# Kernel tuning notes

Hardware: AMD Instinct MI355X
Metric: run time of the kernel (lower is better)

## Reference

```python
import jax, jax.numpy as jnp
import numpy as np

B, S, D_IN = 16, 1024, 1024
H, D_OUT = 16, 128

def setup_inputs() -> dict:
    key = jax.random.key(0)
    k1, k2, k3 = jax.random.split(key, 3)
    x = jax.random.normal(k1, (B, S, D_IN), dtype=jnp.float32)
    W = jax.random.normal(k2, (H, 3, D_IN, D_OUT), dtype=jnp.float32) * (1.0 / np.sqrt(D_IN))
    Wo = jax.random.normal(k3, (H * D_OUT, D_OUT), dtype=jnp.float32) * (1.0 / np.sqrt(H * D_OUT))
    return {"x": x, "W": W, "Wo": Wo}

def reference(x, W, Wo):
    # x: [B,S,D_IN], W: [H,3,D_IN,E], Wo: [H*E,E]
    E = W.shape[-1]
    q = jnp.einsum('bsd,hde->bhse', x, W[:, 0])
    k = jnp.einsum('bsd,hde->bhse', x, W[:, 1])
    v = jnp.einsum('bsd,hde->bhse', x, W[:, 2])
    # NOTE: source divides by (output_dim * 0.5), not sqrt(output_dim)
    scores = jnp.einsum('bhse,bhte->bhst', q, k) / (E * 0.5)
    attn = jax.nn.softmax(scores, axis=-1)
    o = jnp.einsum('bhst,bhte->bhse', attn, v)          # [B,H,S,E]
    o = jnp.transpose(o, (0, 2, 1, 3)).reshape(x.shape[0], x.shape[1], -1)  # concat heads
    return jnp.einsum('bsf,fe->bse', o, Wo)
```

## Files before the change

kernel.cpp:

```cpp
#include <hip/hip_runtime.h>

typedef unsigned short u16;
typedef _Float16 f16;
typedef __attribute__((ext_vector_type(8))) _Float16 half8;
typedef __attribute__((ext_vector_type(8))) short short8;
typedef __attribute__((ext_vector_type(4))) float f32x4;
typedef __attribute__((ext_vector_type(4))) float f4;
typedef __attribute__((ext_vector_type(4))) u16 u16x4;

#define B_ 16
#define S_ 1024
#define DIN_ 1024
#define H_ 16
#define E_ 128

#define EXPK 0.0225546041776533f

__device__ __forceinline__ u16 f2h(float f) {
  f16 h = (f16)f;
  return __builtin_bit_cast(u16, h);
}

__device__ __forceinline__ void gl2lds16(const u16* g, u16* l) {
  __builtin_amdgcn_global_load_lds((const __attribute__((address_space(1))) void*)g,
                                   (__attribute__((address_space(3))) void*)l, 16, 0, 0);
}

__global__ __launch_bounds__(256) void zero_f32(float* __restrict__ p) {
  int i = (blockIdx.x * 256 + threadIdx.x) * 4;
  f4 z = {0.f, 0.f, 0.f, 0.f};
  *reinterpret_cast<f4*>(p + i) = z;
}

__global__ __launch_bounds__(256) void cvt_f32_f16(const float* __restrict__ in,
                                                   u16* __restrict__ out) {
  int i = (blockIdx.x * 256 + threadIdx.x) * 4;
  f4 v = *reinterpret_cast<const f4*>(in + i);
  u16x4 o;
  o[0] = f2h(v[0]); o[1] = f2h(v[1]); o[2] = f2h(v[2]); o[3] = f2h(v[3]);
  *reinterpret_cast<u16x4*>(out + i) = o;
}

__global__ __launch_bounds__(256) void transpose_cvt(const float* __restrict__ in,
                                                     u16* __restrict__ out,
                                                     int R, int C) {
  __shared__ float tile[32][33];
  const size_t moff = (size_t)blockIdx.z * R * C;
  const float* src = in + moff;
  u16* dst = out + moff;
  int c0 = blockIdx.x * 32, r0 = blockIdx.y * 32;
  int tx = threadIdx.x & 31, ty = threadIdx.x >> 5;
#pragma unroll
  for (int i = 0; i < 32; i += 8)
    tile[ty + i][tx] = src[(size_t)(r0 + ty + i) * C + c0 + tx];
  __syncthreads();
#pragma unroll
  for (int i = 0; i < 32; i += 8)
    dst[(size_t)(c0 + ty + i) * R + r0 + tx] = f2h(tile[tx][ty + i]);
}

template<int K>
__global__ __launch_bounds__(512, 2) void gemm256_qkv(const u16* __restrict__ A,
                                                      const u16* __restrict__ BT,
                                                      u16* __restrict__ q, u16* __restrict__ kk,
                                                      u16* __restrict__ vT) {
  constexpr int KT = K / 64;
  const int tid = threadIdx.x;
  const int m0 = blockIdx.x * 256;
  const int nt0 = blockIdx.y;
  const u16* Bblk = BT + (size_t)nt0 * 256 * K;
  __shared__ __align__(16) u16 smem[65536];
  const int w = tid >> 6, lane = tid & 63;
  const int quad = lane >> 4, ln = lane & 15;
  const int wr = w >> 2, wc = w & 3;

  const int srow = tid >> 3;
  const int scc = (tid & 7) ^ (srow & 7);
  const u16* agp = A + (size_t)(m0 + srow) * K + scc * 8;
  const u16* bgp = Bblk + (size_t)srow * K + scc * 8;

#define STAGE256(buf, t)                                                     \
  do {                                                                       \
    u16* ab_ = smem + (buf) * 32768;                                         \
    _Pragma("unroll") for (int i_ = 0; i_ < 4; i_++) {                       \
      gl2lds16(agp + (t) * 64 + (size_t)i_ * 64 * K, ab_ + i_ * 4096 + tid * 8);        \
      gl2lds16(bgp + (t) * 64 + (size_t)i_ * 64 * K, ab_ + 16384 + i_ * 4096 + tid * 8);\
    }                                                                        \
  } while (0)

  int offA[8][2], offB[4][2];
#pragma unroll
  for (int mt = 0; mt < 8; mt++) {
    int row = wr * 128 + mt * 16 + ln;
#pragma unroll
    for (int k2 = 0; k2 < 2; k2++)
      offA[mt][k2] = row * 64 + (((k2 * 4 + quad) ^ (ln & 7)) * 8);
  }
#pragma unroll
  for (int nt = 0; nt < 4; nt++) {
    int row = wc * 64 + nt * 16 + ln;
#pragma unroll
    for (int k2 = 0; k2 < 2; k2++)
      offB[nt][k2] = 16384 + row * 64 + (((k2 * 4 + quad) ^ (ln & 7)) * 8);
  }

  f32x4 acc[8][4];
  f32x4 zero = {0.f, 0.f, 0.f, 0.f};
#pragma unroll
  for (int mt = 0; mt < 8; mt++)
#pragma unroll
    for (int nt = 0; nt < 4; nt++) acc[mt][nt] = zero;

  STAGE256(0, 0);
#pragma unroll
  for (int t = 0; t < KT; t++) {
    asm volatile("s_waitcnt vmcnt(0)" ::: "memory");
    asm volatile("s_barrier" ::: "memory");
    if (t < KT - 1) STAGE256((t + 1) & 1, t + 1);
    const u16* ab = smem + (t & 1) * 32768;
#pragma unroll
    for (int k2 = 0; k2 < 2; k2++) {
      half8 bf[4];
#pragma unroll
      for (int j = 0; j < 4; j++)
        bf[j] = *reinterpret_cast<const half8*>(&ab[offB[j][k2]]);
#pragma unroll
      for (int mh = 0; mh < 2; mh++) {
        half8 af[4];
#pragma unroll
        for (int i = 0; i < 4; i++)
          af[i] = *reinterpret_cast<const half8*>(&ab[offA[mh * 4 + i][k2]]);
        asm volatile("s_barrier" ::: "memory");
        asm volatile("s_waitcnt lgkmcnt(0)" ::: "memory");
        __builtin_amdgcn_sched_barrier(0);
        __builtin_amdgcn_s_setprio(1);
#pragma unroll
        for (int i = 0; i < 4; i++)
#pragma unroll
          for (int j = 0; j < 4; j++)
            acc[mh * 4 + i][j] = __builtin_amdgcn_mfma_f32_16x16x32_f16(
                af[i], bf[j], acc[mh * 4 + i][j], 0, 0, 0);
        __builtin_amdgcn_s_setprio(0);
        asm volatile("s_barrier" ::: "memory");
      }
    }
  }
#undef STAGE256

  __syncthreads();
  const int slab = nt0 * 2 + (wc >> 1);
  const int h = slab / 3, c = slab % 3;
  if (c < 2) {
    u16* dst = (c == 0) ? q : kk;
    const float sc = (c == 0) ? EXPK : 1.0f;
#pragma unroll
    for (int mt = 0; mt < 8; mt++)
#pragma unroll
      for (int nt = 0; nt < 4; nt++)
#pragma unroll
        for (int r = 0; r < 4; r++) {
          int tok = m0 + wr * 128 + mt * 16 + quad * 4 + r;
          int bb = tok >> 10, s = tok & 1023;
          int e = (wc & 1) * 64 + nt * 16 + ln;
          dst[(((size_t)bb * H_ + h) * S_ + s) * E_ + e] = f2h(acc[mt][nt][r] * sc);
        }
  } else {
#pragma unroll
    for (int mt = 0; mt < 8; mt++)
#pragma unroll
      for (int nt = 0; nt < 4; nt++) {
        int tok0 = wr * 128 + mt * 16 + quad * 4;
        int ptok0 = (tok0 & ~31) | ((tok0 & 12) << 1) | ((tok0 & 16) >> 2);
        int e = (wc & 1) * 64 + nt * 16 + ln;
        u16x4 pp;
#pragma unroll
        for (int r = 0; r < 4; r++) pp[r] = f2h(acc[mt][nt][r]);
        *reinterpret_cast<u16x4*>(&smem[e * 260 + ptok0]) = pp;
      }
  }
  __syncthreads();
  int vslab = -1;
  if ((nt0 * 2) % 3 == 2) vslab = 0;
  else if ((nt0 * 2 + 1) % 3 == 2) vslab = 1;
  if (vslab >= 0) {
    const int hv = (nt0 * 2 + vslab) / 3;
    const int bb = m0 >> 10, sbase = m0 & 1023;
    u16* vbase = vT + (((size_t)bb * H_ + hv) * E_) * S_;
#pragma unroll
    for (int i = 0; i < 8; i++) {
      int e = (tid >> 5) + i * 16, s0 = (tid & 31) * 8;
      *reinterpret_cast<short8*>(&vbase[(size_t)e * S_ + sbase + s0]) =
          *reinterpret_cast<const short8*>(&smem[e * 260 + s0]);
    }
  }
}

template<int MODE, int KSPLIT, int K>
__global__ __launch_bounds__(256) void gemm_bt(const u16* __restrict__ A,
                                               const u16* __restrict__ BT,
                                               u16* __restrict__ q, u16* __restrict__ kk,
                                               u16* __restrict__ vT, float* __restrict__ out) {
  const int tid = threadIdx.x;
  const int m0 = blockIdx.x * 128;
  const u16* Bblk = BT + (size_t)blockIdx.y * 128 * K;
  __shared__ __align__(16) u16 smem[132 * 128];
  u16* As = smem;
  u16* Bs = smem + 8192;
  const int w = tid >> 6, lane = tid & 63;
  const int quad = lane >> 4, ln = lane & 15;
  const int wr = w >> 1, wc = w & 1;

  const int kbeg = (KSPLIT > 1) ? blockIdx.z * (K / KSPLIT) : 0;
  constexpr int KLEN = K / KSPLIT;

  const int rr = lane >> 3;
  const int cc = (lane & 7) ^ rr;
  const u16* agp[4];
  const u16* bgp[4];
#pragma unroll
  for (int i = 0; i < 4; i++) {
    int row = i * 32 + w * 8 + rr;
    agp[i] = A + (size_t)(m0 + row) * K + kbeg + cc * 8;
    bgp[i] = Bblk + (size_t)row * K + kbeg + cc * 8;
  }

  int offA[4][2], offB[4][2];
#pragma unroll
  for (int mt = 0; mt < 4; mt++) {
    int row = wr * 64 + mt * 16 + ln;
#pragma unroll
    for (int k2 = 0; k2 < 2; k2++)
      offA[mt][k2] = row * 64 + (((k2 * 4 + quad) ^ (ln & 7)) * 8);
  }
#pragma unroll
  for (int nt = 0; nt < 4; nt++) {
    int row = wc * 64 + nt * 16 + ln;
#pragma unroll
    for (int k2 = 0; k2 < 2; k2++)
      offB[nt][k2] = row * 64 + (((k2 * 4 + quad) ^ (ln & 7)) * 8);
  }

  f32x4 acc[4][4];
  f32x4 zero = {0.f, 0.f, 0.f, 0.f};
#pragma unroll
  for (int mt = 0; mt < 4; mt++)
#pragma unroll
    for (int nt = 0; nt < 4; nt++) acc[mt][nt] = zero;

#pragma unroll
  for (int k0 = 0; k0 < KLEN; k0 += 64) {
    __syncthreads();
#pragma unroll
    for (int i = 0; i < 4; i++) {
      gl2lds16(agp[i] + k0, As + i * 2048 + w * 512);
      gl2lds16(bgp[i] + k0, Bs + i * 2048 + w * 512);
    }
    __syncthreads();
#pragma unroll
    for (int k2 = 0; k2 < 2; k2++) {
      half8 af[4], bfr[4];
#pragma unroll
      for (int mt = 0; mt < 4; mt++)
        af[mt] = *reinterpret_cast<const half8*>(&As[offA[mt][k2]]);
#pragma unroll
      for (int nt = 0; nt < 4; nt++)
        bfr[nt] = *reinterpret_cast<const half8*>(&Bs[offB[nt][k2]]);
#pragma unroll
      for (int mt = 0; mt < 4; mt++)
#pragma unroll
        for (int nt = 0; nt < 4; nt++)
          acc[mt][nt] = __builtin_amdgcn_mfma_f32_16x16x32_f16(af[mt], bfr[nt], acc[mt][nt], 0, 0, 0);
    }
  }

  {
#pragma unroll
    for (int mt = 0; mt < 4; mt++)
#pragma unroll
      for (int nt = 0; nt < 4; nt++)
#pragma unroll
        for (int r = 0; r < 4; r++) {
          int row = wr * 64 + mt * 16 + quad * 4 + r;
          int e = wc * 64 + nt * 16 + ln;
          if (KSPLIT > 1)
            atomicAdd(&out[(size_t)(m0 + row) * E_ + e], acc[mt][nt][r]);
          else
            out[(size_t)(m0 + row) * E_ + e] = acc[mt][nt][r];
        }
  }
}

struct SmemKV {
  u16 ks[64 * 128];
  u16 vs[128 * 64];
};
union SmemAttn {
  u16 qs[128 * 132];
  SmemKV s;
};

__global__ __launch_bounds__(256, 3) void attn_kernel(const u16* __restrict__ qg,
                                                      const u16* __restrict__ kg,
                                                      const u16* __restrict__ vg,
                                                      u16* __restrict__ og) {
  __shared__ __align__(16) SmemAttn sm;
  const int tid = threadIdx.x;
  const int id = blockIdx.x;
  const int g = id >> 6, qt = (id >> 3) & 7, x = id & 7;
  const int hb = g * 8 + x;
  const int b = hb >> 4, h = hb & 15;
  const int q0 = qt * 128;
  const size_t bh = (size_t)(b * H_ + h);
  const u16* qp = qg + bh * S_ * E_;
  const u16* kp = kg + bh * S_ * E_;
  const u16* vp = vg + bh * E_ * S_;
  const int w = tid >> 6, lane = tid & 63, quad = lane >> 4, ln = lane & 15;

#pragma unroll
  for (int i = 0; i < 8; i++) {
    int idx = tid + i * 256;
    int row = idx >> 4, col = (idx & 15) * 8;
    *reinterpret_cast<short8*>(&sm.qs[row * 132 + col]) =
        *reinterpret_cast<const short8*>(&qp[(size_t)(q0 + row) * E_ + col]);
  }
  __syncthreads();
  half8 qf[2][4];
#pragma unroll
  for (int mt = 0; mt < 2; mt++)
#pragma unroll
    for (int ks = 0; ks < 4; ks++)
      qf[mt][ks] = *reinterpret_cast<const half8*>(
          &sm.qs[(w * 32 + mt * 16 + ln) * 132 + ks * 32 + quad * 8]);

  const int krow = w * 4 + (lane >> 4);
  const int kc = ((lane & 15) & 8) | (((lane & 15) & 7) ^ (krow & 7));
  const u16* kbase = kp + (size_t)krow * E_ + kc * 8;
  const int vrow = w * 8 + (lane >> 3);
  const int vc = (lane & 7) ^ ((lane >> 3) & 7);
  const u16* vbase = vp + (size_t)vrow * S_ + vc * 8;

  f32x4 zero = {0.f, 0.f, 0.f, 0.f};
  f32x4 oa[2][8];
#pragma unroll
  for (int mt = 0; mt < 2; mt++)
#pragma unroll
    for (int nt = 0; nt < 8; nt++) oa[mt][nt] = zero;
  float lsum[2] = {0.f, 0.f};

  for (int kt = 0; kt < 16; kt++) {
    __syncthreads();
#pragma unroll
    for (int i = 0; i < 4; i++) {
      gl2lds16(kbase + (size_t)kt * 8192 + i * 16 * E_, &sm.s.ks[(i * 256 + w * 64) * 8]);
      gl2lds16(vbase + (size_t)kt * 64 + i * 32 * S_,   &sm.s.vs[(i * 256 + w * 64) * 8]);
    }
    __syncthreads();

    f32x4 sa[2][4];
#pragma unroll
    for (int mt = 0; mt < 2; mt++)
#pragma unroll
      for (int nt = 0; nt < 4; nt++) sa[mt][nt] = zero;
#pragma unroll
    for (int ks = 0; ks < 4; ks++) {
      half8 kf[4];
#pragma unroll
      for (int nt = 0; nt < 4; nt++) {
        int c = ks * 4 + quad;
        int cs = (c & 8) | ((c & 7) ^ (ln & 7));
        kf[nt] = *reinterpret_cast<const half8*>(&sm.s.ks[(nt * 16 + ln) * 128 + cs * 8]);
      }
#pragma unroll
      for (int mt = 0; mt < 2; mt++)
#pragma unroll
        for (int nt = 0; nt < 4; nt++)
          sa[mt][nt] = __builtin_amdgcn_mfma_f32_16x16x32_f16(kf[nt], qf[mt][ks], sa[mt][nt], 0, 0, 0);
    }

    half8 pfr[2][2];
#pragma unroll
    for (int mt = 0; mt < 2; mt++) {
      float psum = 0.f;
#pragma unroll
      for (int k2 = 0; k2 < 2; k2++) {
        half8 ph;
#pragma unroll
        for (int hhalf = 0; hhalf < 2; hhalf++)
#pragma unroll
          for (int r = 0; r < 4; r++) {
            float p = exp2f(sa[mt][k2 * 2 + hhalf][r]);
            psum += p;
            ph[hhalf * 4 + r] = (f16)p;
          }
        pfr[mt][k2] = ph;
      }
      lsum[mt] += psum;
    }

#pragma unroll
    for (int k2 = 0; k2 < 2; k2++) {
#pragma unroll
      for (int nt8 = 0; nt8 < 8; nt8++) {
        int c = k2 * 4 + quad;
        int cs = c ^ (ln & 7);
        half8 vf = *reinterpret_cast<const half8*>(&sm.s.vs[(nt8 * 16 + ln) * 64 + cs * 8]);
#pragma unroll
        for (int mt = 0; mt < 2; mt++)
          oa[mt][nt8] = __builtin_amdgcn_mfma_f32_16x16x32_f16(pfr[mt][k2], vf, oa[mt][nt8], 0, 0, 0);
      }
    }
  }

#pragma unroll
  for (int mt = 0; mt < 2; mt++) {
    float l = lsum[mt];
    l += __shfl_xor(l, 16);
    l += __shfl_xor(l, 32);
#pragma unroll
    for (int r = 0; r < 4; r++) {
      float lr = __shfl(l, quad * 4 + r);
      float rl = 1.0f / lr;
      int srow = q0 + w * 32 + mt * 16 + quad * 4 + r;
      size_t base = ((size_t)b * S_ + srow) * (H_ * E_) + (size_t)h * E_;
#pragma unroll
      for (int nt8 = 0; nt8 < 8; nt8++)
        og[base + nt8 * 16 + ln] = f2h(oa[mt][nt8][r] * rl);
    }
  }
}

extern "C" void kernel_launch(void* const* d_in, const int* in_sizes, int n_in,
                              void* d_out, int out_size, void* d_ws, size_t ws_size,
                              hipStream_t stream) {
  const float* x = (const float*)d_in[0];
  const float* W = (const float*)d_in[1];
  const float* Wo = (const float*)d_in[2];
  float* out = (float*)d_out;
  char* ws = (char*)d_ws;

  const size_t WBT_BYTES = (size_t)H_ * 3 * DIN_ * E_ * 2;
  const size_t WOT_BYTES = (size_t)H_ * E_ * E_ * 2 * 2;
  const size_t FIXED = WBT_BYTES + WOT_BYTES;

  const size_t XB_PER   = (size_t)S_ * DIN_ * 2;
  const size_t QKV_PER  = (size_t)H_ * S_ * E_ * 2;
  const size_t OB_PER   = (size_t)S_ * H_ * E_ * 2;
  const size_t PER_ITEM = XB_PER + 3 * QKV_PER + OB_PER;

  int Bc = 1;
  for (int c = 16; c >= 1; c >>= 1) {
    if (FIXED + (size_t)c * PER_ITEM <= ws_size) { Bc = c; break; }
  }

  u16* WbT = (u16*)(ws);
  u16* WoT = (u16*)(ws + WBT_BYTES);
  char* cb = ws + FIXED;
  u16* xb  = (u16*)(cb);
  u16* qb  = (u16*)(cb + (size_t)Bc * XB_PER);
  u16* kb  = (u16*)(cb + (size_t)Bc * (XB_PER + QKV_PER));
  u16* vTb = (u16*)(cb + (size_t)Bc * (XB_PER + 2 * QKV_PER));
  u16* ob  = (u16*)(cb + (size_t)Bc * (XB_PER + 3 * QKV_PER));

  zero_f32<<<out_size / 1024, 256, 0, stream>>>(out);
  transpose_cvt<<<dim3(4, 32, 48), 256, 0, stream>>>(W, WbT, DIN_, E_);
  transpose_cvt<<<dim3(4, 64, 1), 256, 0, stream>>>(Wo, WoT, H_ * E_, E_);

  for (int b0 = 0; b0 < B_; b0 += Bc) {
    const float* xc = x + (size_t)b0 * S_ * DIN_;
    cvt_f32_f16<<<Bc * S_ * DIN_ / 1024, 256, 0, stream>>>(xc, xb);
    gemm256_qkv<DIN_><<<dim3(Bc * 4, 24), 512, 0, stream>>>(xb, WbT, qb, kb, vTb);
    attn_kernel<<<Bc * 128, 256, 0, stream>>>(qb, kb, vTb, ob);
    gemm_bt<1, 4, H_ * E_><<<dim3(Bc * 8, 1, 4), 256, 0, stream>>>(ob, WoT, nullptr, nullptr,
                                                                   nullptr, out + (size_t)b0 * S_ * E_);
  }
}
```

Measured before the change: 536.1 us.

## Double-buffer K/V tiles in attention kernel to overlap loads with MFMA

Replaces the single K/V LDS buffer with two buffers. The next tile is prefetched via global_load_lds while the current tile is being computed, and the loop uses one waitcnt plus barrier per iteration instead of two syncthreads. LDS use rises from about 33KB to 64KB per block. That may cut occupancy below the 3 blocks per CU the launch bounds target, trading latency hiding for fewer resident waves.

```diff
diff --git a/kernel.cpp b/kernel.cpp
--- a/kernel.cpp
+++ b/kernel.cpp
@@ -290,20 +290,18 @@
   }
 }
 
-struct SmemKV {
-  u16 ks[64 * 128];
-  u16 vs[128 * 64];
-};
-union SmemAttn {
-  u16 qs[128 * 132];
-  SmemKV s;
+struct SmemAttnDB {
+  union {
+    u16 qs[128 * 132];
+    u16 kv[2][16384];
+  };
 };
 
 __global__ __launch_bounds__(256, 3) void attn_kernel(const u16* __restrict__ qg,
                                                       const u16* __restrict__ kg,
                                                       const u16* __restrict__ vg,
                                                       u16* __restrict__ og) {
-  __shared__ __align__(16) SmemAttn sm;
+  __shared__ __align__(16) SmemAttnDB sm;
   const int tid = threadIdx.x;
   const int id = blockIdx.x;
   const int g = id >> 6, qt = (id >> 3) & 7, x = id & 7;
@@ -331,6 +329,7 @@
     for (int ks = 0; ks < 4; ks++)
       qf[mt][ks] = *reinterpret_cast<const half8*>(
           &sm.qs[(w * 32 + mt * 16 + ln) * 132 + ks * 32 + quad * 8]);
+  __syncthreads();
 
   const int krow = w * 4 + (lane >> 4);
   const int kc = ((lane & 15) & 8) | (((lane & 15) & 7) ^ (krow & 7));
@@ -347,14 +346,28 @@
     for (int nt = 0; nt < 8; nt++) oa[mt][nt] = zero;
   float lsum[2] = {0.f, 0.f};
 
+#pragma unroll
+  for (int i = 0; i < 4; i++) {
+    gl2lds16(kbase + i * 16 * E_, &sm.kv[0][(i * 256 + w * 64) * 8]);
+    gl2lds16(vbase + i * 32 * S_, &sm.kv[0][8192 + (i * 256 + w * 64) * 8]);
+  }
+  asm volatile("s_waitcnt vmcnt(0)" ::: "memory");
+  asm volatile("s_barrier" ::: "memory");
+
   for (int kt = 0; kt < 16; kt++) {
-    __syncthreads();
-#pragma unroll
-    for (int i = 0; i < 4; i++) {
-      gl2lds16(kbase + (size_t)kt * 8192 + i * 16 * E_, &sm.s.ks[(i * 256 + w * 64) * 8]);
-      gl2lds16(vbase + (size_t)kt * 64 + i * 32 * S_,   &sm.s.vs[(i * 256 + w * 64) * 8]);
-    }
-    __syncthreads();
+    const int cur = kt & 1;
+    if (kt < 15) {
+      const int nxt = cur ^ 1;
+#pragma unroll
+      for (int i = 0; i < 4; i++) {
+        gl2lds16(kbase + (size_t)(kt + 1) * 8192 + i * 16 * E_,
+                 &sm.kv[nxt][(i * 256 + w * 64) * 8]);
+        gl2lds16(vbase + (size_t)(kt + 1) * 64 + i * 32 * S_,
+                 &sm.kv[nxt][8192 + (i * 256 + w * 64) * 8]);
+      }
+    }
+    const u16* ksr = &sm.kv[cur][0];
+    const u16* vsr = &sm.kv[cur][8192];
 
     f32x4 sa[2][4];
 #pragma unroll
@@ -368,7 +381,7 @@
       for (int nt = 0; nt < 4; nt++) {
         int c = ks * 4 + quad;
         int cs = (c & 8) | ((c & 7) ^ (ln & 7));
-        kf[nt] = *reinterpret_cast<const half8*>(&sm.s.ks[(nt * 16 + ln) * 128 + cs * 8]);
+        kf[nt] = *reinterpret_cast<const half8*>(&ksr[(nt * 16 + ln) * 128 + cs * 8]);
       }
 #pragma unroll
       for (int mt = 0; mt < 2; mt++)
@@ -403,11 +416,16 @@
       for (int nt8 = 0; nt8 < 8; nt8++) {
         int c = k2 * 4 + quad;
         int cs = c ^ (ln & 7);
-        half8 vf = *reinterpret_cast<const half8*>(&sm.s.vs[(nt8 * 16 + ln) * 64 + cs * 8]);
+        half8 vf = *reinterpret_cast<const half8*>(&vsr[(nt8 * 16 + ln) * 64 + cs * 8]);
 #pragma unroll
         for (int mt = 0; mt < 2; mt++)
           oa[mt][nt8] = __builtin_amdgcn_mfma_f32_16x16x32_f16(pfr[mt][k2], vf, oa[mt][nt8], 0, 0, 0);
       }
+    }
+
+    if (kt < 15) {
+      asm volatile("s_waitcnt vmcnt(0)" ::: "memory");
+      asm volatile("s_barrier" ::: "memory");
     }
   }
 
```

Result: no change. 546.3 us (+1.9%).

## Load QKV GEMM B operand directly into registers, stage only A in LDS

Applied to the files above, without the earlier changes.

In the QKV projection GEMM, the weight (B) tiles are no longer staged through LDS. Each wave loads its B fragments straight from global memory into registers, with a register double buffer for the next K step. LDS shrinks to about half and now holds only the A tiles. The intra-step s_barrier/lgkmcnt/sched_barrier fences around the MFMA blocks are also removed. This cuts LDS traffic and barriers and may allow higher occupancy, but B is now read redundantly by the waves sharing a column and uses more VGPRs, which could cause spills.

```diff
diff --git a/kernel.cpp b/kernel.cpp
--- a/kernel.cpp
+++ b/kernel.cpp
@@ -69,7 +69,7 @@
   const int m0 = blockIdx.x * 256;
   const int nt0 = blockIdx.y;
   const u16* Bblk = BT + (size_t)nt0 * 256 * K;
-  __shared__ __align__(16) u16 smem[65536];
+  __shared__ __align__(16) u16 smem[33536];
   const int w = tid >> 6, lane = tid & 63;
   const int quad = lane >> 4, ln = lane & 15;
   const int wr = w >> 2, wc = w & 3;
@@ -77,18 +77,22 @@
   const int srow = tid >> 3;
   const int scc = (tid & 7) ^ (srow & 7);
   const u16* agp = A + (size_t)(m0 + srow) * K + scc * 8;
-  const u16* bgp = Bblk + (size_t)srow * K + scc * 8;
-
-#define STAGE256(buf, t)                                                     \
+
+#define STAGE_A(buf, t)                                                      \
   do {                                                                       \
-    u16* ab_ = smem + (buf) * 32768;                                         \
-    _Pragma("unroll") for (int i_ = 0; i_ < 4; i_++) {                       \
-      gl2lds16(agp + (t) * 64 + (size_t)i_ * 64 * K, ab_ + i_ * 4096 + tid * 8);        \
-      gl2lds16(bgp + (t) * 64 + (size_t)i_ * 64 * K, ab_ + 16384 + i_ * 4096 + tid * 8);\
-    }                                                                        \
+    u16* ab_ = smem + (buf) * 16384;                                         \
+    _Pragma("unroll") for (int i_ = 0; i_ < 4; i_++)                         \
+      gl2lds16(agp + (t) * 64 + (size_t)i_ * 64 * K, ab_ + i_ * 4096 + tid * 8); \
   } while (0)
 
-  int offA[8][2], offB[4][2];
+  const u16* bp[4][2];
+#pragma unroll
+  for (int nt = 0; nt < 4; nt++)
+#pragma unroll
+    for (int k2 = 0; k2 < 2; k2++)
+      bp[nt][k2] = Bblk + (size_t)(wc * 64 + nt * 16 + ln) * K + k2 * 32 + quad * 8;
+
+  int offA[8][2];
 #pragma unroll
   for (int mt = 0; mt < 8; mt++) {
     int row = wr * 128 + mt * 16 + ln;
@@ -96,13 +100,6 @@
     for (int k2 = 0; k2 < 2; k2++)
       offA[mt][k2] = row * 64 + (((k2 * 4 + quad) ^ (ln & 7)) * 8);
   }
-#pragma unroll
-  for (int nt = 0; nt < 4; nt++) {
-    int row = wc * 64 + nt * 16 + ln;
-#pragma unroll
-    for (int k2 = 0; k2 < 2; k2++)
-      offB[nt][k2] = 16384 + row * 64 + (((k2 * 4 + quad) ^ (ln & 7)) * 8);
-  }
 
   f32x4 acc[8][4];
   f32x4 zero = {0.f, 0.f, 0.f, 0.f};
@@ -111,41 +108,55 @@
 #pragma unroll
     for (int nt = 0; nt < 4; nt++) acc[mt][nt] = zero;
 
-  STAGE256(0, 0);
+  STAGE_A(0, 0);
+  half8 bcur[2][4];
+#pragma unroll
+  for (int k2 = 0; k2 < 2; k2++)
+#pragma unroll
+    for (int nt = 0; nt < 4; nt++)
+      bcur[k2][nt] = *reinterpret_cast<const half8*>(bp[nt][k2]);
+
 #pragma unroll
   for (int t = 0; t < KT; t++) {
     asm volatile("s_waitcnt vmcnt(0)" ::: "memory");
     asm volatile("s_barrier" ::: "memory");
-    if (t < KT - 1) STAGE256((t + 1) & 1, t + 1);
-    const u16* ab = smem + (t & 1) * 32768;
+    half8 bnxt[2][4];
+    if (t < KT - 1) {
+      STAGE_A((t + 1) & 1, t + 1);
+#pragma unroll
+      for (int k2 = 0; k2 < 2; k2++)
+#pragma unroll
+        for (int nt = 0; nt < 4; nt++)
+          bnxt[k2][nt] = *reinterpret_cast<const half8*>(bp[nt][k2] + (t + 1) * 64);
+    }
+    const u16* ab = smem + (t & 1) * 16384;
 #pragma unroll
     for (int k2 = 0; k2 < 2; k2++) {
-      half8 bf[4];
-#pragma unroll
-      for (int j = 0; j < 4; j++)
-        bf[j] = *reinterpret_cast<const half8*>(&ab[offB[j][k2]]);
 #pragma unroll
       for (int mh = 0; mh < 2; mh++) {
         half8 af[4];
 #pragma unroll
         for (int i = 0; i < 4; i++)
           af[i] = *reinterpret_cast<const half8*>(&ab[offA[mh * 4 + i][k2]]);
-        asm volatile("s_barrier" ::: "memory");
-        asm volatile("s_waitcnt lgkmcnt(0)" ::: "memory");
-        __builtin_amdgcn_sched_barrier(0);
         __builtin_amdgcn_s_setprio(1);
 #pragma unroll
         for (int i = 0; i < 4; i++)
 #pragma unroll
           for (int j = 0; j < 4; j++)
             acc[mh * 4 + i][j] = __builtin_amdgcn_mfma_f32_16x16x32_f16(
-                af[i], bf[j], acc[mh * 4 + i][j], 0, 0, 0);
+                af[i], bcur[k2][j], acc[mh * 4 + i][j], 0, 0, 0);
         __builtin_amdgcn_s_setprio(0);
-        asm volatile("s_barrier" ::: "memory");
       }
     }
-  }
-#undef STAGE256
+    if (t < KT - 1) {
+#pragma unroll
+      for (int k2 = 0; k2 < 2; k2++)
+#pragma unroll
+        for (int nt = 0; nt < 4; nt++)
+          bcur[k2][nt] = bnxt[k2][nt];
+    }
+  }
+#undef STAGE_A
 
   __syncthreads();
   const int slab = nt0 * 2 + (wc >> 1);
```

New measurement: 616.0 us. 1.15x slower.
